# Kernel optimization log

Measured on AMD Instinct MI355X. Metric: run time of the kernel, lower is better.

Reference implementation:

```python
import jax, jax.numpy as jnp
import numpy as np

T, B, NN = 20, 4, 500            # timesteps, batch, nodes per sample
M = B * NN                        # big-batched node count = 2000
IN_D, H, H2, OUT = 2, 128, 64, 32


def setup_inputs() -> dict:
    key = jax.random.key(0)
    ks = jax.random.split(key, 16)
    positions = jax.random.normal(ks[0], (T, M, IN_D), jnp.float32)
    adjacency = (jax.random.uniform(ks[1], (T, M, M)) < 0.01).astype(jnp.float32)
    adjacency = adjacency * (1.0 - jnp.eye(M, dtype=jnp.float32))
    ego_mask = jax.random.bernoulli(ks[2], 0.8, (B, T, NN))
    s = lambda k, shp, fan: (jax.random.normal(k, shp, jnp.float32) / np.sqrt(fan)).astype(jnp.float32)
    return {
        'positions': positions,
        'adjacency': adjacency,
        'ego_mask': ego_mask,
        'W1': s(ks[3], (IN_D, H), IN_D), 'b1': jnp.zeros((H,), jnp.float32),
        'W2': s(ks[4], (H, H), H),       'b2': jnp.zeros((H,), jnp.float32),
        'W_ih': s(ks[5], (4 * H, H), H), 'W_hh': s(ks[6], (4 * H, H), H),
        'b_ih': jnp.zeros((4 * H,), jnp.float32), 'b_hh': jnp.zeros((4 * H,), jnp.float32),
        'fc1_w': s(ks[7], (H, H2), H),   'fc1_b': jnp.zeros((H2,), jnp.float32),
        'fc2_w': s(ks[8], (H2, OUT), H2), 'fc2_b': jnp.zeros((OUT,), jnp.float32),
    }


def _forward(positions, adjacency, ego_mask, W1, b1, W2, b2,
             W_ih, W_hh, b_ih, b_hh, fc1_w, fc1_b, fc2_w, fc2_b):
    # ego_mask [B,T,NN] -> [T, B*NN] (matches permute(1,0,2).reshape(T,-1))
    mask = jnp.transpose(ego_mask, (1, 0, 2)).reshape(T, M).astype(positions.dtype)

    def gcn_timestep(x_t, a_t, m_t):
        # masked subgraph + self loops on kept nodes (PyG GCNConv normalization)
        Ahat = a_t * m_t[:, None] * m_t[None, :] + jnp.diag(m_t)   # [M,M]
        deg = Ahat.sum(axis=0)                                      # in-degree (col sum)
        dinv = jnp.where(deg > 0, jax.lax.rsqrt(jnp.maximum(deg, 1e-12)), 0.0)
        An = dinv[:, None] * Ahat * dinv[None, :]                   # D^-1/2 Ahat D^-1/2
        h1 = jax.nn.relu(An.T @ (x_t @ W1) + b1)                    # GCN1 + relu
        h2 = (An.T @ (h1 @ W2) + b2) * m_t[:, None]                 # GCN2, scatter into zeros
        return h2

    placeholder = jax.vmap(gcn_timestep)(positions, adjacency, mask)  # [T, M, H]

    # torch nn.LSTM (batch_first=False) on placeholder.transpose(0,1):
    # sequence axis = nodes (M), batch axis = T
    xs = jnp.transpose(placeholder, (1, 0, 2))  # [M, T, H]

    def lstm_step(carry, x_s):
        h, c = carry
        gates = x_s @ W_ih.T + b_ih + h @ W_hh.T + b_hh
        i, f, g, o = jnp.split(gates, 4, axis=-1)
        c = jax.nn.sigmoid(f) * c + jax.nn.sigmoid(i) * jnp.tanh(g)
        h = jax.nn.sigmoid(o) * jnp.tanh(c)
        return (h, c), h

    init = (jnp.zeros((T, H), positions.dtype), jnp.zeros((T, H), positions.dtype))
    _, lstm_out = jax.lax.scan(lstm_step, init, xs)  # [M, T, H]

    emb = lstm_out.reshape(B, NN, T, H)              # view(B, max_nodes, T, H)
    emb = jax.nn.relu(emb @ fc1_w + fc1_b)
    return emb @ fc2_w + fc2_b                       # [B, NN, T, OUT]


def reference(positions, adjacency, ego_mask, W1, b1, W2, b2,
              W_ih, W_hh, b_ih, b_hh, fc1_w, fc1_b, fc2_w, fc2_b):
    return _forward(positions, adjacency, ego_mask, W1, b1, W2, b2,
                    W_ih, W_hh, b_ih, b_hh, fc1_w, fc1_b, fc2_w, fc2_b)
```

## Files before the change

kernel.cpp:

```cpp
#include <hip/hip_runtime.h>
#include <hip/hip_bf16.h>

#define T_   20
#define B_   4
#define NN_  500
#define M_   2000
#define TM_  40000
#define H_   128
#define G_   512
#define H2_  64
#define OUT_ 32
#define ECAP 64
#define TG_  (T_ * G_)

typedef unsigned short ushort_t;
typedef unsigned int   uint_t;
typedef _Float16       f16;
typedef f16 f16x2 __attribute__((ext_vector_type(2)));
typedef f16 f16x8 __attribute__((ext_vector_type(8)));
typedef float f32x4 __attribute__((ext_vector_type(4)));

#if defined(__has_builtin)
#  if __has_builtin(__builtin_amdgcn_fdot2)
#    define HAVE_FDOT2 1
#  endif
#endif

__device__ inline float fdot2_(f16x2 a, f16x2 b, float c) {
#ifdef HAVE_FDOT2
    return __builtin_amdgcn_fdot2(a, b, c, false);
#else
    return c + (float)a.x * (float)b.x + (float)a.y * (float)b.y;
#endif
}

__device__ inline float fast_sig(float x) {
    float e = __builtin_amdgcn_exp2f(x * -1.4426950408889634f);
    return __builtin_amdgcn_rcpf(1.f + e);
}
__device__ inline float fast_tanh(float x) {
    float e = __builtin_amdgcn_exp2f(x * 2.8853900817779268f);
    return 1.f - 2.f * __builtin_amdgcn_rcpf(e + 1.f);
}

#define BARRAW() asm volatile("s_barrier" ::: "memory")

__global__ __launch_bounds__(1024) void k0_mask(const void* __restrict__ ego,
                                                float* __restrict__ mf,
                                                int* __restrict__ ecnt) {
    __shared__ int fl[3];
    int tid = threadIdx.x;
    if (tid < 3) fl[tid] = 0;
    __syncthreads();
    const uint_t* dw = (const uint_t*)ego;
    int a = 0, b = 0, c = 0;
    for (int i = tid; i < 2500; i += 1024) {
        uint_t v = dw[i];
        bool isf32  = (v == 0x3F800000u);
        bool isbf16 = (v == 0x00003F80u) || (v == 0x3F803F80u);
        if (isf32)  a = 1;
        if (isbf16) b = 1;
        if (v > 1u && !isf32 && !isbf16) c = 1;
    }
    if (a) fl[0] = 1;
    if (b) fl[1] = 1;
    if (c) fl[2] = 1;
    __syncthreads();
    int mode;
    if (fl[1])      mode = 3;
    else if (fl[0]) mode = 2;
    else if (fl[2]) mode = 1;
    else            mode = 0;
    int e = blockIdx.x * 1024 + tid;
    if (e >= TM_) return;
    ecnt[e] = 0;
    int t = e / M_, i = e % M_;
    int bb = i / NN_, n = i % NN_;
    int src = (bb * T_ + t) * NN_ + n;
    bool on;
    if (mode == 0)      on = ((const int*)ego)[src] != 0;
    else if (mode == 1) on = ((const unsigned char*)ego)[src] != 0;
    else if (mode == 2) on = ((const float*)ego)[src] != 0.f;
    else                on = ((const ushort_t*)ego)[src] != 0;
    mf[e] = on ? 1.f : 0.f;
}

#define JSTRIP 200
__global__ void k1_scan(const float* __restrict__ adj, const float* __restrict__ mf,
                        int* __restrict__ ecnt, int* __restrict__ edges) {
    __shared__ float ms[JSTRIP];
    int t = blockIdx.y, j0 = blockIdx.z * JSTRIP;
    int i = blockIdx.x * 256 + threadIdx.x;
    for (int idx = threadIdx.x; idx < JSTRIP; idx += 256)
        ms[idx] = mf[t * M_ + j0 + idx];
    __syncthreads();
    if (i >= M_) return;
    if (mf[t * M_ + i] == 0.f) return;
    const float* ap = adj + (size_t)t * M_ * M_ + (size_t)j0 * M_ + i;
    int r = t * M_ + i;
    int* ep = edges + (size_t)r * ECAP;
#pragma unroll 8
    for (int jj = 0; jj < JSTRIP; ++jj) {
        float av = ap[(size_t)jj * M_];
        if (av != 0.f && ms[jj] != 0.f) {
            int pos = atomicAdd(&ecnt[r], 1);
            if (pos < ECAP) ep[pos] = j0 + jj;
        }
    }
}

__global__ void k2_y1(const float* __restrict__ pos, const float* __restrict__ W1,
                      const float* __restrict__ mf, const int* __restrict__ ecnt,
                      float* __restrict__ dinv, f16* __restrict__ Y1) {
    int gid = blockIdx.x * 256 + threadIdx.x;
    int r = gid >> 7, h = gid & 127;
    if (r >= TM_) return;
    float mr = mf[r];
    int cnt = ecnt[r];
    float dv = (mr != 0.f) ? __frsqrt_rn((float)(cnt + 1)) : 0.f;
    if (h == 0) dinv[r] = dv;
    float2 xy = ((const float2*)pos)[r];
    float v = xy.x * W1[h] + xy.y * W1[H_ + h];
    Y1[gid] = (f16)(dv * v);
}

__global__ __launch_bounds__(64) void k3_agg1(const f16* __restrict__ Y1,
        const float* __restrict__ dinv, const int* __restrict__ ecnt,
        const int* __restrict__ edges, const float* __restrict__ b1,
        f16* __restrict__ h1) {
    int r = blockIdx.x, q = threadIdx.x;
    int t = r / M_, base = t * M_;
    const uint_t* Yu = (const uint_t*)Y1;
    f16x2 sp = __builtin_bit_cast(f16x2, Yu[(size_t)r * 64 + q]);
    float a0 = (float)sp.x, a1 = (float)sp.y;
    int ec = ecnt[r]; if (ec > ECAP) ec = ECAP;
    const int4* ep4 = (const int4*)(edges + (size_t)r * ECAP);
    for (int e = 0; e < ec; e += 4) {
        int4 ix = ep4[e >> 2];
        int j1 = (e + 1 < ec) ? ix.y : ix.x;
        int j2 = (e + 2 < ec) ? ix.z : ix.x;
        int j3 = (e + 3 < ec) ? ix.w : ix.x;
        uint_t u0 = Yu[(size_t)(base + ix.x) * 64 + q];
        uint_t u1 = Yu[(size_t)(base + j1) * 64 + q];
        uint_t u2 = Yu[(size_t)(base + j2) * 64 + q];
        uint_t u3 = Yu[(size_t)(base + j3) * 64 + q];
        f16x2 p0 = __builtin_bit_cast(f16x2, u0);
        a0 += (float)p0.x; a1 += (float)p0.y;
        if (e + 1 < ec) { f16x2 p = __builtin_bit_cast(f16x2, u1); a0 += (float)p.x; a1 += (float)p.y; }
        if (e + 2 < ec) { f16x2 p = __builtin_bit_cast(f16x2, u2); a0 += (float)p.x; a1 += (float)p.y; }
        if (e + 3 < ec) { f16x2 p = __builtin_bit_cast(f16x2, u3); a0 += (float)p.x; a1 += (float)p.y; }
    }
    float dv = dinv[r];
    float o0 = dv * a0 + b1[2 * q];
    float o1 = dv * a1 + b1[2 * q + 1];
    f16x2 op; op.x = (f16)fmaxf(o0, 0.f); op.y = (f16)fmaxf(o1, 0.f);
    ((uint_t*)h1)[(size_t)r * 64 + q] = __builtin_bit_cast(uint_t, op);
}

__global__ __launch_bounds__(64) void k5_agg2(const f16* __restrict__ Y2,
        const float* __restrict__ dinv, const float* __restrict__ mf,
        const int* __restrict__ ecnt, const int* __restrict__ edges,
        const float* __restrict__ b2, f16* __restrict__ ph) {
    int r = blockIdx.x, q = threadIdx.x;
    int t = r / M_, base = t * M_;
    const uint_t* Yu = (const uint_t*)Y2;
    f16x2 sp = __builtin_bit_cast(f16x2, Yu[(size_t)r * 64 + q]);
    float a0 = (float)sp.x, a1 = (float)sp.y;
    int ec = ecnt[r]; if (ec > ECAP) ec = ECAP;
    const int4* ep4 = (const int4*)(edges + (size_t)r * ECAP);
    for (int e = 0; e < ec; e += 4) {
        int4 ix = ep4[e >> 2];
        int j1 = (e + 1 < ec) ? ix.y : ix.x;
        int j2 = (e + 2 < ec) ? ix.z : ix.x;
        int j3 = (e + 3 < ec) ? ix.w : ix.x;
        uint_t u0 = Yu[(size_t)(base + ix.x) * 64 + q];
        uint_t u1 = Yu[(size_t)(base + j1) * 64 + q];
        uint_t u2 = Yu[(size_t)(base + j2) * 64 + q];
        uint_t u3 = Yu[(size_t)(base + j3) * 64 + q];
        f16x2 p0 = __builtin_bit_cast(f16x2, u0);
        a0 += (float)p0.x; a1 += (float)p0.y;
        if (e + 1 < ec) { f16x2 p = __builtin_bit_cast(f16x2, u1); a0 += (float)p.x; a1 += (float)p.y; }
        if (e + 2 < ec) { f16x2 p = __builtin_bit_cast(f16x2, u2); a0 += (float)p.x; a1 += (float)p.y; }
        if (e + 3 < ec) { f16x2 p = __builtin_bit_cast(f16x2, u3); a0 += (float)p.x; a1 += (float)p.y; }
    }
    float dv = dinv[r], mr = mf[r];
    f16x2 op;
    op.x = (f16)((dv * a0 + b2[2 * q]) * mr);
    op.y = (f16)((dv * a1 + b2[2 * q + 1]) * mr);
    ((uint_t*)ph)[(size_t)r * 64 + q] = __builtin_bit_cast(uint_t, op);
}

#define ALD 136
__global__ __launch_bounds__(256) void kgemm_mfma(const f16* __restrict__ A,
        const float* __restrict__ Bw, int bTrans, int Ntot, int mode,
        const float* __restrict__ dinv, const float* __restrict__ ba,
        const float* __restrict__ bb, f16* __restrict__ Out) {
    __shared__ f16 As[64 * ALD];
    __shared__ f16 Bs[64 * ALD];
    int m0 = blockIdx.x * 64;
    int n0 = blockIdx.y * 64;
    int tid = threadIdx.x;
#pragma unroll
    for (int u = 0; u < 4; ++u) {
        int idx = u * 256 + tid;
        int row = idx >> 4, seg = idx & 15;
        *(f16x8*)&As[row * ALD + seg * 8] =
            *(const f16x8*)(A + (size_t)(m0 + row) * H_ + seg * 8);
    }
    if (bTrans) {
#pragma unroll
        for (int u = 0; u < 16; ++u) {
            int idx = u * 256 + tid;
            int n = idx >> 6, k2 = (idx & 63) * 2;
            float2 v = *(const float2*)(Bw + (size_t)(n0 + n) * H_ + k2);
            f16x2 pk; pk.x = (f16)v.x; pk.y = (f16)v.y;
            *(uint_t*)&Bs[n * ALD + k2] = __builtin_bit_cast(uint_t, pk);
        }
    } else {
#pragma unroll
        for (int u = 0; u < 16; ++u) {
            int idx = u * 256 + tid;
            int n = idx >> 6, k2 = (idx & 63) * 2;
            f16x2 pk;
            pk.x = (f16)Bw[(size_t)k2 * Ntot + n0 + n];
            pk.y = (f16)Bw[(size_t)(k2 + 1) * Ntot + n0 + n];
            *(uint_t*)&Bs[n * ALD + k2] = __builtin_bit_cast(uint_t, pk);
        }
    }
    __syncthreads();
    int w = tid >> 6, lane = tid & 63;
    int col = lane & 15, quad = lane >> 4;
    f32x4 acc[4] = {};
#pragma unroll
    for (int kk = 0; kk < 4; ++kk) {
        f16x8 af = *(const f16x8*)&As[(w * 16 + col) * ALD + kk * 32 + quad * 8];
#pragma unroll
        for (int nt = 0; nt < 4; ++nt) {
            f16x8 bf = *(const f16x8*)&Bs[(nt * 16 + col) * ALD + kk * 32 + quad * 8];
            acc[nt] = __builtin_amdgcn_mfma_f32_16x16x32_f16(af, bf, acc[nt], 0, 0, 0);
        }
    }
    if (mode == 0) {
        float dv[4];
#pragma unroll
        for (int reg = 0; reg < 4; ++reg)
            dv[reg] = dinv[m0 + w * 16 + quad * 4 + reg];
#pragma unroll
        for (int nt = 0; nt < 4; ++nt) {
            int n = n0 + nt * 16 + col;
#pragma unroll
            for (int reg = 0; reg < 4; ++reg) {
                int r = m0 + w * 16 + quad * 4 + reg;
                Out[(size_t)r * Ntot + n] = (f16)(dv[reg] * acc[nt][reg]);
            }
        }
    } else {
#pragma unroll
        for (int nt = 0; nt < 4; ++nt) {
            int n = n0 + nt * 16 + col;
            float bias = ba[n] + bb[n];
#pragma unroll
            for (int reg = 0; reg < 4; ++reg) {
                int r = m0 + w * 16 + quad * 4 + reg;
                int t = r / M_, s = r % M_;
                Out[((size_t)s * T_ + t) * G_ + n] = (f16)(acc[nt][reg] + bias);
            }
        }
    }
}

__global__ __launch_bounds__(512, 2) void k7_lstm(const float* __restrict__ Whh,
        const f16* __restrict__ xg, f16* __restrict__ lo) {
    __shared__ uint_t hb2[2][H_ / 2];
    int t = blockIdx.x, tid = threadIdx.x;
    int h = tid >> 2, q = tid & 3;
    f16x2 w0[16], w1[16], w2[16], w3[16];
    {
        const float* base = Whh + (size_t)h * H_ + q * 32;
#pragma unroll
        for (int d = 0; d < 16; ++d) {
            f16x2 p;
            p.x = (f16)base[0 * G_ * 32 + 2 * d];
            p.y = (f16)base[0 * G_ * 32 + 2 * d + 1];
            w0[d] = p;
            p.x = (f16)base[(size_t)H_ * H_ + 2 * d];
            p.y = (f16)base[(size_t)H_ * H_ + 2 * d + 1];
            w1[d] = p;
            p.x = (f16)base[(size_t)2 * H_ * H_ + 2 * d];
            p.y = (f16)base[(size_t)2 * H_ * H_ + 2 * d + 1];
            w2[d] = p;
            p.x = (f16)base[(size_t)3 * H_ * H_ + 2 * d];
            p.y = (f16)base[(size_t)3 * H_ * H_ + 2 * d + 1];
            w3[d] = p;
        }
    }
    if (tid < H_ / 2) hb2[0][tid] = 0;
    float cst = 0.f;
    const ushort_t* xpu = (const ushort_t*)xg + t * G_ + q * H_ + h;
    ushort_t xa[8], xb[8];
#pragma unroll
    for (int k = 0; k < 8; ++k) xa[k] = xpu[(size_t)k * TG_];
    __syncthreads();

#define LSTM_STEP(S, XV)                                                      \
    do {                                                                      \
        const uint4* hbp = (const uint4*)&hb2[(S) & 1][0];                    \
        float a0 = 0.f, a1 = 0.f, a2 = 0.f, a3 = 0.f;                         \
        _Pragma("unroll")                                                     \
        for (int d = 0; d < 4; ++d) {                                         \
            uint4 hv = hbp[q * 4 + d];                                        \
            f16x2 e0 = __builtin_bit_cast(f16x2, hv.x);                       \
            f16x2 e1 = __builtin_bit_cast(f16x2, hv.y);                       \
            f16x2 e2 = __builtin_bit_cast(f16x2, hv.z);                       \
            f16x2 e3 = __builtin_bit_cast(f16x2, hv.w);                       \
            a0 = fdot2_(w0[4 * d + 3], e3, fdot2_(w0[4 * d + 2], e2,          \
                 fdot2_(w0[4 * d + 1], e1, fdot2_(w0[4 * d + 0], e0, a0))));  \
            a1 = fdot2_(w1[4 * d + 3], e3, fdot2_(w1[4 * d + 2], e2,          \
                 fdot2_(w1[4 * d + 1], e1, fdot2_(w1[4 * d + 0], e0, a1))));  \
            a2 = fdot2_(w2[4 * d + 3], e3, fdot2_(w2[4 * d + 2], e2,          \
                 fdot2_(w2[4 * d + 1], e1, fdot2_(w2[4 * d + 0], e0, a2))));  \
            a3 = fdot2_(w3[4 * d + 3], e3, fdot2_(w3[4 * d + 2], e2,          \
                 fdot2_(w3[4 * d + 1], e1, fdot2_(w3[4 * d + 0], e0, a3))));  \
        }                                                                     \
        float xf = (float)__builtin_bit_cast(f16, (ushort_t)(XV));            \
        a0 += (q == 0) ? xf : 0.f;                                            \
        a1 += (q == 1) ? xf : 0.f;                                            \
        a2 += (q == 2) ? xf : 0.f;                                            \
        a3 += (q == 3) ? xf : 0.f;                                            \
        a0 += __shfl_xor(a0, 1); a0 += __shfl_xor(a0, 2);                     \
        a1 += __shfl_xor(a1, 1); a1 += __shfl_xor(a1, 2);                     \
        a2 += __shfl_xor(a2, 1); a2 += __shfl_xor(a2, 2);                     \
        a3 += __shfl_xor(a3, 1); a3 += __shfl_xor(a3, 2);                     \
        float gi = fast_sig(a0), gf = fast_sig(a1);                           \
        float gg = fast_tanh(a2), go = fast_sig(a3);                          \
        cst = gf * cst + gi * gg;                                             \
        float hv_ = go * fast_tanh(cst);                                      \
        if (q == 0) {                                                         \
            f16 hh = (f16)hv_;                                                \
            ((ushort_t*)&hb2[((S) & 1) ^ 1][0])[h] =                          \
                __builtin_bit_cast(ushort_t, hh);                             \
            lo[((size_t)(S) * T_ + t) * H_ + h] = hh;                         \
        }                                                                     \
        BARRAW();                                                             \
    } while (0)

    for (int c2 = 0; c2 < 125; ++c2) {
        int sA = c2 * 16;
#pragma unroll
        for (int k = 0; k < 8; ++k) xb[k] = xpu[(size_t)(sA + 8 + k) * TG_];
#pragma unroll
        for (int k = 0; k < 8; ++k) LSTM_STEP(sA + k, xa[k]);
        int nbs = (sA + 16 <= M_ - 8) ? sA + 16 : M_ - 8;
#pragma unroll
        for (int k = 0; k < 8; ++k) xa[k] = xpu[(size_t)(nbs + k) * TG_];
#pragma unroll
        for (int k = 0; k < 8; ++k) LSTM_STEP(sA + 8 + k, xb[k]);
    }
#undef LSTM_STEP
}

__global__ __launch_bounds__(256) void k8_fc(const f16* __restrict__ lo,
        const float* __restrict__ w1, const float* __restrict__ fb1,
        const float* __restrict__ w2, const float* __restrict__ fb2,
        float* __restrict__ out) {
    __shared__ uint_t hl[4][H_ / 2];
    __shared__ float o1f[4][H2_];
    int tid = threadIdx.x;
    int o = tid & 63, rr = tid >> 6;
    f16x2 w1c[64];
#pragma unroll
    for (int d = 0; d < 64; ++d) {
        f16x2 p;
        p.x = (f16)w1[(2 * d) * H2_ + o];
        p.y = (f16)w1[(2 * d + 1) * H2_ + o];
        w1c[d] = p;
    }
    int o2 = o & 31;
    float w2f[64];
#pragma unroll
    for (int d = 0; d < 64; ++d) w2f[d] = w2[d * OUT_ + o2];
    float fb1v = fb1[o], fb2v = fb2[o2];

    for (int r0 = blockIdx.x * 4; r0 < TM_; r0 += 512 * 4) {
        {
            int row = tid >> 6, qq = tid & 63;
            hl[row][qq] = ((const uint_t*)lo)[(size_t)(r0 + row) * 64 + qq];
        }
        __syncthreads();
        float acc = fb1v;
        const uint4* hb = (const uint4*)&hl[rr][0];
#pragma unroll
        for (int d = 0; d < 16; ++d) {
            uint4 hv = hb[d];
            acc = fdot2_(w1c[4 * d + 0], __builtin_bit_cast(f16x2, hv.x), acc);
            acc = fdot2_(w1c[4 * d + 1], __builtin_bit_cast(f16x2, hv.y), acc);
            acc = fdot2_(w1c[4 * d + 2], __builtin_bit_cast(f16x2, hv.z), acc);
            acc = fdot2_(w1c[4 * d + 3], __builtin_bit_cast(f16x2, hv.w), acc);
        }
        o1f[rr][o] = fmaxf(acc, 0.f);
        __syncthreads();
        if (o < OUT_) {
            float a2 = fb2v;
            const float4* ob = (const float4*)&o1f[rr][0];
#pragma unroll
            for (int d = 0; d < 16; ++d) {
                float4 v = ob[d];
                a2 += v.x * w2f[4 * d + 0] + v.y * w2f[4 * d + 1]
                    + v.z * w2f[4 * d + 2] + v.w * w2f[4 * d + 3];
            }
            out[(size_t)(r0 + rr) * OUT_ + o] = a2;
        }
        __syncthreads();
    }
}

extern "C" void kernel_launch(void* const* d_in, const int* in_sizes, int n_in,
                              void* d_out, int out_size, void* d_ws, size_t ws_size,
                              hipStream_t stream) {
    const float* positions = (const float*)d_in[0];
    const float* adjacency = (const float*)d_in[1];
    const void*  ego       = d_in[2];
    const float* W1   = (const float*)d_in[3];
    const float* b1   = (const float*)d_in[4];
    const float* W2   = (const float*)d_in[5];
    const float* b2   = (const float*)d_in[6];
    const float* W_ih = (const float*)d_in[7];
    const float* W_hh = (const float*)d_in[8];
    const float* b_ih = (const float*)d_in[9];
    const float* b_hh = (const float*)d_in[10];
    const float* fc1w = (const float*)d_in[11];
    const float* fc1b = (const float*)d_in[12];
    const float* fc2w = (const float*)d_in[13];
    const float* fc2b = (const float*)d_in[14];
    float* out = (float*)d_out;

    char* p = (char*)d_ws;
    auto alloc = [&](size_t bytes) {
        void* r = (void*)p;
        p += (bytes + 255) & ~(size_t)255;
        return r;
    };
    float* mf    = (float*)alloc((size_t)TM_ * 4);
    float* dinv  = (float*)alloc((size_t)TM_ * 4);
    int*   ecnt  = (int*)alloc((size_t)TM_ * 4);
    int*   edges = (int*)alloc((size_t)TM_ * ECAP * 4);
    f16*   bufC  = (f16*)alloc((size_t)TM_ * H_ * 2);
    f16*   bufD  = (f16*)alloc((size_t)TM_ * H_ * 2);
    f16*   xg    = (f16*)alloc((size_t)TM_ * G_ * 2);
    f16*   Y1 = bufC, *Y2 = bufC;
    f16*   h1 = bufD, *ph = bufD;
    f16*   lo = (f16*)edges;

    hipLaunchKernelGGL(k0_mask, dim3(40), dim3(1024), 0, stream, ego, mf, ecnt);
    hipLaunchKernelGGL(k1_scan, dim3(8, 20, 10), dim3(256), 0, stream,
                       adjacency, mf, ecnt, edges);
    hipLaunchKernelGGL(k2_y1, dim3(20000), dim3(256), 0, stream,
                       positions, W1, mf, ecnt, dinv, Y1);
    hipLaunchKernelGGL(k3_agg1, dim3(40000), dim3(64), 0, stream,
                       Y1, dinv, ecnt, edges, b1, h1);
    hipLaunchKernelGGL(kgemm_mfma, dim3(625, 2), dim3(256), 0, stream,
                       h1, W2, 0, 128, 0, dinv, (const float*)nullptr,
                       (const float*)nullptr, Y2);
    hipLaunchKernelGGL(k5_agg2, dim3(40000), dim3(64), 0, stream,
                       Y2, dinv, mf, ecnt, edges, b2, ph);
    hipLaunchKernelGGL(kgemm_mfma, dim3(625, 8), dim3(256), 0, stream,
                       ph, W_ih, 1, 512, 1, dinv, b_ih, b_hh, xg);
    hipLaunchKernelGGL(k7_lstm, dim3(20), dim3(512), 0, stream, W_hh, xg, lo);
    hipLaunchKernelGGL(k8_fc, dim3(512), dim3(256), 0, stream,
                       lo, fc1w, fc1b, fc2w, fc2b, out);
}
```

Before: 1.918 ms.

## Restructure LSTM recurrence to two gate rows per thread with 256 threads

The LSTM kernel now uses 256 threads per block. Each thread pair owns one hidden unit, and each thread computes two full 128-long gate rows (i,f or g,o) from register-resident weights, so the four-lane shuffle reduction is no longer needed. The xg GEMM epilogue now interleaves the gate columns so each thread loads both of its input gate values with one 32-bit read. This halves the threads per block and removes the reduction shuffles on the serial critical path. In exchange each thread does twice the dot-product work and holds 128 weight registers, which raises register pressure.

```diff
diff --git a/kernel.cpp b/kernel.cpp
--- a/kernel.cpp
+++ b/kernel.cpp
@@ -259,102 +259,122 @@
         for (int nt = 0; nt < 4; ++nt) {
             int n = n0 + nt * 16 + col;
             float bias = ba[n] + bb[n];
+            int pos = (n & 127) * 4 + (n >> 7);
 #pragma unroll
             for (int reg = 0; reg < 4; ++reg) {
                 int r = m0 + w * 16 + quad * 4 + reg;
                 int t = r / M_, s = r % M_;
-                Out[((size_t)s * T_ + t) * G_ + n] = (f16)(acc[nt][reg] + bias);
+                Out[((size_t)s * T_ + t) * G_ + pos] = (f16)(acc[nt][reg] + bias);
             }
         }
     }
 }
 
-__global__ __launch_bounds__(512, 2) void k7_lstm(const float* __restrict__ Whh,
+__global__ __launch_bounds__(256, 1) void k7_lstm(const float* __restrict__ Whh,
         const f16* __restrict__ xg, f16* __restrict__ lo) {
     __shared__ uint_t hb2[2][H_ / 2];
     int t = blockIdx.x, tid = threadIdx.x;
-    int h = tid >> 2, q = tid & 3;
-    f16x2 w0[16], w1[16], w2[16], w3[16];
+    int m = tid >> 1, p = tid & 1;
+    int n1 = p ? (2 * H_ + m) : m;
+    int n2 = n1 + H_;
+    f16x2 wA[64], wB[64];
     {
-        const float* base = Whh + (size_t)h * H_ + q * 32;
-#pragma unroll
-        for (int d = 0; d < 16; ++d) {
-            f16x2 p;
-            p.x = (f16)base[0 * G_ * 32 + 2 * d];
-            p.y = (f16)base[0 * G_ * 32 + 2 * d + 1];
-            w0[d] = p;
-            p.x = (f16)base[(size_t)H_ * H_ + 2 * d];
-            p.y = (f16)base[(size_t)H_ * H_ + 2 * d + 1];
-            w1[d] = p;
-            p.x = (f16)base[(size_t)2 * H_ * H_ + 2 * d];
-            p.y = (f16)base[(size_t)2 * H_ * H_ + 2 * d + 1];
-            w2[d] = p;
-            p.x = (f16)base[(size_t)3 * H_ * H_ + 2 * d];
-            p.y = (f16)base[(size_t)3 * H_ * H_ + 2 * d + 1];
-            w3[d] = p;
+        const float* rA = Whh + (size_t)n1 * H_;
+        const float* rB = Whh + (size_t)n2 * H_;
+#pragma unroll
+        for (int d = 0; d < 64; ++d) {
+            f16x2 a, b;
+            a.x = (f16)rA[2 * d]; a.y = (f16)rA[2 * d + 1];
+            b.x = (f16)rB[2 * d]; b.y = (f16)rB[2 * d + 1];
+            wA[d] = a; wB[d] = b;
         }
     }
     if (tid < H_ / 2) hb2[0][tid] = 0;
     float cst = 0.f;
-    const ushort_t* xpu = (const ushort_t*)xg + t * G_ + q * H_ + h;
-    ushort_t xa[8], xb[8];
-#pragma unroll
-    for (int k = 0; k < 8; ++k) xa[k] = xpu[(size_t)k * TG_];
+    const uint_t* xpu = (const uint_t*)xg + t * (G_ / 2) + m * 2 + p;
+    uint_t xa[8], xb[8];
+#pragma unroll
+    for (int k = 0; k < 8; ++k) xa[k] = xpu[(size_t)k * (TG_ / 2)];
     __syncthreads();
 
 #define LSTM_STEP(S, XV)                                                      \
     do {                                                                      \
         const uint4* hbp = (const uint4*)&hb2[(S) & 1][0];                    \
-        float a0 = 0.f, a1 = 0.f, a2 = 0.f, a3 = 0.f;                         \
+        float cA0 = 0.f, cA1 = 0.f, cA2 = 0.f, cA3 = 0.f;                     \
+        float cB0 = 0.f, cB1 = 0.f, cB2 = 0.f, cB3 = 0.f;                     \
         _Pragma("unroll")                                                     \
         for (int d = 0; d < 4; ++d) {                                         \
-            uint4 hv = hbp[q * 4 + d];                                        \
-            f16x2 e0 = __builtin_bit_cast(f16x2, hv.x);                       \
-            f16x2 e1 = __builtin_bit_cast(f16x2, hv.y);                       \
-            f16x2 e2 = __builtin_bit_cast(f16x2, hv.z);                       \
-            f16x2 e3 = __builtin_bit_cast(f16x2, hv.w);                       \
-            a0 = fdot2_(w0[4 * d + 3], e3, fdot2_(w0[4 * d + 2], e2,          \
-                 fdot2_(w0[4 * d + 1], e1, fdot2_(w0[4 * d + 0], e0, a0))));  \
-            a1 = fdot2_(w1[4 * d + 3], e3, fdot2_(w1[4 * d + 2], e2,          \
-                 fdot2_(w1[4 * d + 1], e1, fdot2_(w1[4 * d + 0], e0, a1))));  \
-            a2 = fdot2_(w2[4 * d + 3], e3, fdot2_(w2[4 * d + 2], e2,          \
-                 fdot2_(w2[4 * d + 1], e1, fdot2_(w2[4 * d + 0], e0, a2))));  \
-            a3 = fdot2_(w3[4 * d + 3], e3, fdot2_(w3[4 * d + 2], e2,          \
-                 fdot2_(w3[4 * d + 1], e1, fdot2_(w3[4 * d + 0], e0, a3))));  \
+            uint4 h0 = hbp[4 * d + 0];                                        \
+            uint4 h1v = hbp[4 * d + 1];                                       \
+            uint4 h2v = hbp[4 * d + 2];                                       \
+            uint4 h3v = hbp[4 * d + 3];                                       \
+            f16x2 e;                                                          \
+            e = __builtin_bit_cast(f16x2, h0.x);                              \
+            cA0 = fdot2_(wA[16 * d + 0], e, cA0); cB0 = fdot2_(wB[16 * d + 0], e, cB0); \
+            e = __builtin_bit_cast(f16x2, h0.y);                              \
+            cA0 = fdot2_(wA[16 * d + 1], e, cA0); cB0 = fdot2_(wB[16 * d + 1], e, cB0); \
+            e = __builtin_bit_cast(f16x2, h0.z);                              \
+            cA0 = fdot2_(wA[16 * d + 2], e, cA0); cB0 = fdot2_(wB[16 * d + 2], e, cB0); \
+            e = __builtin_bit_cast(f16x2, h0.w);                              \
+            cA0 = fdot2_(wA[16 * d + 3], e, cA0); cB0 = fdot2_(wB[16 * d + 3], e, cB0); \
+            e = __builtin_bit_cast(f16x2, h1v.x);                             \
+            cA1 = fdot2_(wA[16 * d + 4], e, cA1); cB1 = fdot2_(wB[16 * d + 4], e, cB1); \
+            e = __builtin_bit_cast(f16x2, h1v.y);                             \
+            cA1 = fdot2_(wA[16 * d + 5], e, cA1); cB1 = fdot2_(wB[16 * d + 5], e, cB1); \
+            e = __builtin_bit_cast(f16x2, h1v.z);                             \
+            cA1 = fdot2_(wA[16 * d + 6], e, cA1); cB1 = fdot2_(wB[16 * d + 6], e, cB1); \
+            e = __builtin_bit_cast(f16x2, h1v.w);                             \
+            cA1 = fdot2_(wA[16 * d + 7], e, cA1); cB1 = fdot2_(wB[16 * d + 7], e, cB1); \
+            e = __builtin_bit_cast(f16x2, h2v.x);                             \
+            cA2 = fdot2_(wA[16 * d + 8], e, cA2); cB2 = fdot2_(wB[16 * d + 8], e, cB2); \
+            e = __builtin_bit_cast(f16x2, h2v.y);                             \
+            cA2 = fdot2_(wA[16 * d + 9], e, cA2); cB2 = fdot2_(wB[16 * d + 9], e, cB2); \
+            e = __builtin_bit_cast(f16x2, h2v.z);                             \
+            cA2 = fdot2_(wA[16 * d + 10], e, cA2); cB2 = fdot2_(wB[16 * d + 10], e, cB2); \
+            e = __builtin_bit_cast(f16x2, h2v.w);                             \
+            cA2 = fdot2_(wA[16 * d + 11], e, cA2); cB2 = fdot2_(wB[16 * d + 11], e, cB2); \
+            e = __builtin_bit_cast(f16x2, h3v.x);                             \
+            cA3 = fdot2_(wA[16 * d + 12], e, cA3); cB3 = fdot2_(wB[16 * d + 12], e, cB3); \
+            e = __builtin_bit_cast(f16x2, h3v.y);                             \
+            cA3 = fdot2_(wA[16 * d + 13], e, cA3); cB3 = fdot2_(wB[16 * d + 13], e, cB3); \
+            e = __builtin_bit_cast(f16x2, h3v.z);                             \
+            cA3 = fdot2_(wA[16 * d + 14], e, cA3); cB3 = fdot2_(wB[16 * d + 14], e, cB3); \
+            e = __builtin_bit_cast(f16x2, h3v.w);                             \
+            cA3 = fdot2_(wA[16 * d + 15], e, cA3); cB3 = fdot2_(wB[16 * d + 15], e, cB3); \
         }                                                                     \
-        float xf = (float)__builtin_bit_cast(f16, (ushort_t)(XV));            \
-        a0 += (q == 0) ? xf : 0.f;                                            \
-        a1 += (q == 1) ? xf : 0.f;                                            \
-        a2 += (q == 2) ? xf : 0.f;                                            \
-        a3 += (q == 3) ? xf : 0.f;                                            \
-        a0 += __shfl_xor(a0, 1); a0 += __shfl_xor(a0, 2);                     \
-        a1 += __shfl_xor(a1, 1); a1 += __shfl_xor(a1, 2);                     \
-        a2 += __shfl_xor(a2, 1); a2 += __shfl_xor(a2, 2);                     \
-        a3 += __shfl_xor(a3, 1); a3 += __shfl_xor(a3, 2);                     \
-        float gi = fast_sig(a0), gf = fast_sig(a1);                           \
-        float gg = fast_tanh(a2), go = fast_sig(a3);                          \
+        f16x2 xp = __builtin_bit_cast(f16x2, (uint_t)(XV));                   \
+        float sA = (cA0 + cA1) + (cA2 + cA3) + (float)xp.x;                   \
+        float sB = (cB0 + cB1) + (cB2 + cB3) + (float)xp.y;                   \
+        float actA = p ? fast_tanh(sA) : fast_sig(sA);                        \
+        float actB = fast_sig(sB);                                            \
+        float oA = __shfl_xor(actA, 1);                                       \
+        float oB = __shfl_xor(actB, 1);                                       \
+        float gi = p ? oA : actA;                                             \
+        float gf = p ? oB : actB;                                             \
+        float gg = p ? actA : oA;                                             \
+        float go = p ? actB : oB;                                             \
         cst = gf * cst + gi * gg;                                             \
         float hv_ = go * fast_tanh(cst);                                      \
-        if (q == 0) {                                                         \
-            f16 hh = (f16)hv_;                                                \
-            ((ushort_t*)&hb2[((S) & 1) ^ 1][0])[h] =                          \
+        f16 hh = (f16)hv_;                                                    \
+        if (p == 0)                                                           \
+            ((ushort_t*)&hb2[((S) & 1) ^ 1][0])[m] =                          \
                 __builtin_bit_cast(ushort_t, hh);                             \
-            lo[((size_t)(S) * T_ + t) * H_ + h] = hh;                         \
-        }                                                                     \
+        else                                                                  \
+            lo[((size_t)(S) * T_ + t) * H_ + m] = hh;                         \
         BARRAW();                                                             \
     } while (0)
 
     for (int c2 = 0; c2 < 125; ++c2) {
-        int sA = c2 * 16;
-#pragma unroll
-        for (int k = 0; k < 8; ++k) xb[k] = xpu[(size_t)(sA + 8 + k) * TG_];
-#pragma unroll
-        for (int k = 0; k < 8; ++k) LSTM_STEP(sA + k, xa[k]);
-        int nbs = (sA + 16 <= M_ - 8) ? sA + 16 : M_ - 8;
-#pragma unroll
-        for (int k = 0; k < 8; ++k) xa[k] = xpu[(size_t)(nbs + k) * TG_];
-#pragma unroll
-        for (int k = 0; k < 8; ++k) LSTM_STEP(sA + 8 + k, xb[k]);
+        int s0 = c2 * 16;
+#pragma unroll
+        for (int k = 0; k < 8; ++k) xb[k] = xpu[(size_t)(s0 + 8 + k) * (TG_ / 2)];
+#pragma unroll
+        for (int k = 0; k < 8; ++k) LSTM_STEP(s0 + k, xa[k]);
+        int nbs = (s0 + 16 <= M_ - 8) ? s0 + 16 : M_ - 8;
+#pragma unroll
+        for (int k = 0; k < 8; ++k) xa[k] = xpu[(size_t)(nbs + k) * (TG_ / 2)];
+#pragma unroll
+        for (int k = 0; k < 8; ++k) LSTM_STEP(s0 + 8 + k, xb[k]);
     }
 #undef LSTM_STEP
 }
@@ -465,7 +485,7 @@
                        Y2, dinv, mf, ecnt, edges, b2, ph);
     hipLaunchKernelGGL(kgemm_mfma, dim3(625, 8), dim3(256), 0, stream,
                        ph, W_ih, 1, 512, 1, dinv, b_ih, b_hh, xg);
-    hipLaunchKernelGGL(k7_lstm, dim3(20), dim3(512), 0, stream, W_hh, xg, lo);
+    hipLaunchKernelGGL(k7_lstm, dim3(20), dim3(256), 0, stream, W_hh, xg, lo);
     hipLaunchKernelGGL(k8_fc, dim3(512), dim3(256), 0, stream,
                        lo, fc1w, fc1b, fc2w, fc2b, out);
 }
```

New measurement: 1.819 ms. -5.2%, faster.

## Compute LSTM recurrent matvec with MFMA and interleave gate layout

Applied to the files above, without the earlier changes.

The LSTM recurrence kernel replaces per-thread fdot2 dot products and cross-lane shuffle reductions with MFMA 16x16x32 f16 instructions. Each wave owns 16 hidden units and keeps W_hh fragments in registers. The hidden state is broadcast as the A operand, and only row 0 of each result is used. The input-gate projection kernel now writes gates interleaved per hidden unit, so one 8-byte load fetches all four gate preactivations for a unit. This is meant to shorten the serial per-step critical path, at the cost of wasting 15/16 of the MFMA rows and leaving only a quarter of lanes active for the activations.

```diff
diff --git a/kernel.cpp b/kernel.cpp
--- a/kernel.cpp
+++ b/kernel.cpp
@@ -259,11 +259,12 @@
         for (int nt = 0; nt < 4; ++nt) {
             int n = n0 + nt * 16 + col;
             float bias = ba[n] + bb[n];
+            int pos = (n & 127) * 4 + (n >> 7);
 #pragma unroll
             for (int reg = 0; reg < 4; ++reg) {
                 int r = m0 + w * 16 + quad * 4 + reg;
                 int t = r / M_, s = r % M_;
-                Out[((size_t)s * T_ + t) * G_ + n] = (f16)(acc[nt][reg] + bias);
+                Out[((size_t)s * T_ + t) * G_ + pos] = (f16)(acc[nt][reg] + bias);
             }
         }
     }
@@ -271,90 +272,96 @@
 
 __global__ __launch_bounds__(512, 2) void k7_lstm(const float* __restrict__ Whh,
         const f16* __restrict__ xg, f16* __restrict__ lo) {
-    __shared__ uint_t hb2[2][H_ / 2];
+    __shared__ ushort_t hb2[2][H_];
     int t = blockIdx.x, tid = threadIdx.x;
-    int h = tid >> 2, q = tid & 3;
-    f16x2 w0[16], w1[16], w2[16], w3[16];
-    {
-        const float* base = Whh + (size_t)h * H_ + q * 32;
-#pragma unroll
-        for (int d = 0; d < 16; ++d) {
-            f16x2 p;
-            p.x = (f16)base[0 * G_ * 32 + 2 * d];
-            p.y = (f16)base[0 * G_ * 32 + 2 * d + 1];
-            w0[d] = p;
-            p.x = (f16)base[(size_t)H_ * H_ + 2 * d];
-            p.y = (f16)base[(size_t)H_ * H_ + 2 * d + 1];
-            w1[d] = p;
-            p.x = (f16)base[(size_t)2 * H_ * H_ + 2 * d];
-            p.y = (f16)base[(size_t)2 * H_ * H_ + 2 * d + 1];
-            w2[d] = p;
-            p.x = (f16)base[(size_t)3 * H_ * H_ + 2 * d];
-            p.y = (f16)base[(size_t)3 * H_ * H_ + 2 * d + 1];
-            w3[d] = p;
-        }
-    }
-    if (tid < H_ / 2) hb2[0][tid] = 0;
+    int w = tid >> 6, lane = tid & 63;
+    int col16 = lane & 15, quad = lane >> 4;
+    int m = w * 16 + col16;
+    f16x8 wf[4][4];
+#pragma unroll
+    for (int gt = 0; gt < 4; ++gt)
+#pragma unroll
+        for (int kk = 0; kk < 4; ++kk) {
+            const float* wp = Whh + (size_t)(gt * H_ + m) * H_ + kk * 32 + quad * 8;
+            float4 va = *(const float4*)wp;
+            float4 vb = *(const float4*)(wp + 4);
+            f16x8 f;
+            f[0] = (f16)va.x; f[1] = (f16)va.y; f[2] = (f16)va.z; f[3] = (f16)va.w;
+            f[4] = (f16)vb.x; f[5] = (f16)vb.y; f[6] = (f16)vb.z; f[7] = (f16)vb.w;
+            wf[gt][kk] = f;
+        }
+    if (tid < H_) hb2[0][tid] = 0;
     float cst = 0.f;
-    const ushort_t* xpu = (const ushort_t*)xg + t * G_ + q * H_ + h;
-    ushort_t xa[8], xb[8];
-#pragma unroll
-    for (int k = 0; k < 8; ++k) xa[k] = xpu[(size_t)k * TG_];
+    const f32x4 zero4 = {0.f, 0.f, 0.f, 0.f};
+    const uint_t* xbase = (const uint_t*)xg;
+    uint2 xa[4], xb[4];
+    if (quad == 0) {
+#pragma unroll
+        for (int k = 0; k < 4; ++k)
+            xa[k] = *(const uint2*)(xbase + ((size_t)k * T_ + t) * 256 + m * 2);
+    }
     __syncthreads();
 
 #define LSTM_STEP(S, XV)                                                      \
     do {                                                                      \
-        const uint4* hbp = (const uint4*)&hb2[(S) & 1][0];                    \
-        float a0 = 0.f, a1 = 0.f, a2 = 0.f, a3 = 0.f;                         \
-        _Pragma("unroll")                                                     \
-        for (int d = 0; d < 4; ++d) {                                         \
-            uint4 hv = hbp[q * 4 + d];                                        \
-            f16x2 e0 = __builtin_bit_cast(f16x2, hv.x);                       \
-            f16x2 e1 = __builtin_bit_cast(f16x2, hv.y);                       \
-            f16x2 e2 = __builtin_bit_cast(f16x2, hv.z);                       \
-            f16x2 e3 = __builtin_bit_cast(f16x2, hv.w);                       \
-            a0 = fdot2_(w0[4 * d + 3], e3, fdot2_(w0[4 * d + 2], e2,          \
-                 fdot2_(w0[4 * d + 1], e1, fdot2_(w0[4 * d + 0], e0, a0))));  \
-            a1 = fdot2_(w1[4 * d + 3], e3, fdot2_(w1[4 * d + 2], e2,          \
-                 fdot2_(w1[4 * d + 1], e1, fdot2_(w1[4 * d + 0], e0, a1))));  \
-            a2 = fdot2_(w2[4 * d + 3], e3, fdot2_(w2[4 * d + 2], e2,          \
-                 fdot2_(w2[4 * d + 1], e1, fdot2_(w2[4 * d + 0], e0, a2))));  \
-            a3 = fdot2_(w3[4 * d + 3], e3, fdot2_(w3[4 * d + 2], e2,          \
-                 fdot2_(w3[4 * d + 1], e1, fdot2_(w3[4 * d + 0], e0, a3))));  \
-        }                                                                     \
-        float xf = (float)__builtin_bit_cast(f16, (ushort_t)(XV));            \
-        a0 += (q == 0) ? xf : 0.f;                                            \
-        a1 += (q == 1) ? xf : 0.f;                                            \
-        a2 += (q == 2) ? xf : 0.f;                                            \
-        a3 += (q == 3) ? xf : 0.f;                                            \
-        a0 += __shfl_xor(a0, 1); a0 += __shfl_xor(a0, 2);                     \
-        a1 += __shfl_xor(a1, 1); a1 += __shfl_xor(a1, 2);                     \
-        a2 += __shfl_xor(a2, 1); a2 += __shfl_xor(a2, 2);                     \
-        a3 += __shfl_xor(a3, 1); a3 += __shfl_xor(a3, 2);                     \
-        float gi = fast_sig(a0), gf = fast_sig(a1);                           \
-        float gg = fast_tanh(a2), go = fast_sig(a3);                          \
-        cst = gf * cst + gi * gg;                                             \
-        float hv_ = go * fast_tanh(cst);                                      \
-        if (q == 0) {                                                         \
+        const ushort_t* hp = &hb2[(S) & 1][0];                                \
+        uint4 u0 = *(const uint4*)(hp + quad * 8);                            \
+        uint4 u1 = *(const uint4*)(hp + 32 + quad * 8);                       \
+        uint4 u2 = *(const uint4*)(hp + 64 + quad * 8);                       \
+        uint4 u3 = *(const uint4*)(hp + 96 + quad * 8);                       \
+        f16x8 a0 = __builtin_bit_cast(f16x8, u0);                             \
+        f16x8 a1 = __builtin_bit_cast(f16x8, u1);                             \
+        f16x8 a2 = __builtin_bit_cast(f16x8, u2);                             \
+        f16x8 a3 = __builtin_bit_cast(f16x8, u3);                             \
+        f32x4 g0 = __builtin_amdgcn_mfma_f32_16x16x32_f16(a0, wf[0][0], zero4, 0, 0, 0); \
+        f32x4 g1 = __builtin_amdgcn_mfma_f32_16x16x32_f16(a0, wf[1][0], zero4, 0, 0, 0); \
+        f32x4 g2 = __builtin_amdgcn_mfma_f32_16x16x32_f16(a0, wf[2][0], zero4, 0, 0, 0); \
+        f32x4 g3 = __builtin_amdgcn_mfma_f32_16x16x32_f16(a0, wf[3][0], zero4, 0, 0, 0); \
+        g0 = __builtin_amdgcn_mfma_f32_16x16x32_f16(a1, wf[0][1], g0, 0, 0, 0); \
+        g1 = __builtin_amdgcn_mfma_f32_16x16x32_f16(a1, wf[1][1], g1, 0, 0, 0); \
+        g2 = __builtin_amdgcn_mfma_f32_16x16x32_f16(a1, wf[2][1], g2, 0, 0, 0); \
+        g3 = __builtin_amdgcn_mfma_f32_16x16x32_f16(a1, wf[3][1], g3, 0, 0, 0); \
+        g0 = __builtin_amdgcn_mfma_f32_16x16x32_f16(a2, wf[0][2], g0, 0, 0, 0); \
+        g1 = __builtin_amdgcn_mfma_f32_16x16x32_f16(a2, wf[1][2], g1, 0, 0, 0); \
+        g2 = __builtin_amdgcn_mfma_f32_16x16x32_f16(a2, wf[2][2], g2, 0, 0, 0); \
+        g3 = __builtin_amdgcn_mfma_f32_16x16x32_f16(a2, wf[3][2], g3, 0, 0, 0); \
+        g0 = __builtin_amdgcn_mfma_f32_16x16x32_f16(a3, wf[0][3], g0, 0, 0, 0); \
+        g1 = __builtin_amdgcn_mfma_f32_16x16x32_f16(a3, wf[1][3], g1, 0, 0, 0); \
+        g2 = __builtin_amdgcn_mfma_f32_16x16x32_f16(a3, wf[2][3], g2, 0, 0, 0); \
+        g3 = __builtin_amdgcn_mfma_f32_16x16x32_f16(a3, wf[3][3], g3, 0, 0, 0); \
+        if (quad == 0) {                                                      \
+            f16x2 xlo = __builtin_bit_cast(f16x2, (XV).x);                    \
+            f16x2 xhi = __builtin_bit_cast(f16x2, (XV).y);                    \
+            float gi = fast_sig(g0[0] + (float)xlo.x);                        \
+            float gf = fast_sig(g1[0] + (float)xlo.y);                        \
+            float gg = fast_tanh(g2[0] + (float)xhi.x);                       \
+            float go = fast_sig(g3[0] + (float)xhi.y);                        \
+            cst = gf * cst + gi * gg;                                         \
+            float hv_ = go * fast_tanh(cst);                                  \
             f16 hh = (f16)hv_;                                                \
-            ((ushort_t*)&hb2[((S) & 1) ^ 1][0])[h] =                          \
-                __builtin_bit_cast(ushort_t, hh);                             \
-            lo[((size_t)(S) * T_ + t) * H_ + h] = hh;                         \
+            hb2[((S) & 1) ^ 1][m] = __builtin_bit_cast(ushort_t, hh);         \
+            lo[((size_t)(S) * T_ + t) * H_ + m] = hh;                         \
         }                                                                     \
         BARRAW();                                                             \
     } while (0)
 
-    for (int c2 = 0; c2 < 125; ++c2) {
-        int sA = c2 * 16;
-#pragma unroll
-        for (int k = 0; k < 8; ++k) xb[k] = xpu[(size_t)(sA + 8 + k) * TG_];
-#pragma unroll
-        for (int k = 0; k < 8; ++k) LSTM_STEP(sA + k, xa[k]);
-        int nbs = (sA + 16 <= M_ - 8) ? sA + 16 : M_ - 8;
-#pragma unroll
-        for (int k = 0; k < 8; ++k) xa[k] = xpu[(size_t)(nbs + k) * TG_];
-#pragma unroll
-        for (int k = 0; k < 8; ++k) LSTM_STEP(sA + 8 + k, xb[k]);
+    for (int c2 = 0; c2 < 250; ++c2) {
+        int s0 = c2 * 8;
+        if (quad == 0) {
+#pragma unroll
+            for (int k = 0; k < 4; ++k)
+                xb[k] = *(const uint2*)(xbase + ((size_t)(s0 + 4 + k) * T_ + t) * 256 + m * 2);
+        }
+#pragma unroll
+        for (int k = 0; k < 4; ++k) LSTM_STEP(s0 + k, xa[k]);
+        int nbs = (s0 + 8 <= M_ - 4) ? s0 + 8 : M_ - 4;
+        if (quad == 0) {
+#pragma unroll
+            for (int k = 0; k < 4; ++k)
+                xa[k] = *(const uint2*)(xbase + ((size_t)(nbs + k) * T_ + t) * 256 + m * 2);
+        }
+#pragma unroll
+        for (int k = 0; k < 4; ++k) LSTM_STEP(s0 + 4 + k, xb[k]);
     }
 #undef LSTM_STEP
 }
```

New measurement: 1.676 ms. 12.6% less time.
